# Kernel optimization log

Hardware: AMD Instinct MI355X
Metric: run time of the kernel (lower is better)

Reference implementation:

```python
import jax, jax.numpy as jnp
import numpy as np

N = 16384
E = 262144
IN_F, HID, ENC = 3, 128, 768
NEG_SLOPE = 0.2
EPS = 1e-5


def _glorot(key, shape):
    lim = float(np.sqrt(6.0 / (shape[0] + shape[1])))
    return jax.random.uniform(key, shape, jnp.float32, -lim, lim)


def layernorm(x, g, b):
    mu = jnp.mean(x, axis=-1, keepdims=True)
    var = jnp.mean(jnp.square(x - mu), axis=-1, keepdims=True)
    return (x - mu) * jax.lax.rsqrt(var + EPS) * g + b


def gatv2(x, src, dst, Wl, bl, Wr, br, att, bias, n_nodes):
    # single-head GATv2: message = lin_l(x)[src], score from lin_l(x)[src] + lin_r(x)[dst]
    xl = x @ Wl + bl                                  # [N, C]
    xr = x @ Wr + br                                  # [N, C]
    e = jax.nn.leaky_relu(xl[src] + xr[dst], NEG_SLOPE) @ att   # [E]
    m = jax.ops.segment_max(e, dst, num_segments=n_nodes)       # per-dst max (self-loops => no empty segs)
    ex = jnp.exp(e - m[dst])
    denom = jax.ops.segment_sum(ex, dst, num_segments=n_nodes)
    alpha = ex / denom[dst]                           # [E]
    out = jax.ops.segment_sum(alpha[:, None] * xl[src], dst, num_segments=n_nodes)
    return out + bias


def setup_inputs() -> dict:
    key = jax.random.key(0)
    ks = jax.random.split(key, 12)
    x = jax.random.normal(ks[0], (N, IN_F), jnp.float32)
    edge_index = jax.random.randint(ks[1], (2, E), 0, N, jnp.int64)
    return {
        "x": x,
        "edge_index": edge_index,
        "Wfc": _glorot(ks[2], (IN_F, ENC)),
        "bfc": jnp.zeros((ENC,), jnp.float32),
        "W1l": _glorot(ks[3], (IN_F, HID)),
        "b1l": jnp.zeros((HID,), jnp.float32),
        "W1r": _glorot(ks[4], (IN_F, HID)),
        "b1r": jnp.zeros((HID,), jnp.float32),
        "att1": _glorot(ks[5], (HID, 1))[:, 0],
        "bias1": jnp.zeros((HID,), jnp.float32),
        "g_bn1": jnp.ones((HID,), jnp.float32),
        "bb_bn1": jnp.zeros((HID,), jnp.float32),
        "W2l": _glorot(ks[6], (HID, ENC)),
        "b2l": jnp.zeros((ENC,), jnp.float32),
        "W2r": _glorot(ks[7], (HID, ENC)),
        "b2r": jnp.zeros((ENC,), jnp.float32),
        "att2": _glorot(ks[8], (ENC, 1))[:, 0],
        "bias2": jnp.zeros((ENC,), jnp.float32),
        "g_norm": jnp.ones((ENC,), jnp.float32),
        "b_norm": jnp.zeros((ENC,), jnp.float32),
    }


def reference(x, edge_index, Wfc, bfc, W1l, b1l, W1r, b1r, att1, bias1,
              g_bn1, bb_bn1, W2l, b2l, W2r, b2r, att2, bias2, g_norm, b_norm):
    loops = jnp.arange(N, dtype=edge_index.dtype)
    src = jnp.concatenate([edge_index[0], loops])   # add self-loops (PyG default)
    dst = jnp.concatenate([edge_index[1], loops])
    res = x @ Wfc + bfc                              # [N, ENC]
    h = gatv2(x, src, dst, W1l, b1l, W1r, b1r, att1, bias1, N)
    h = jax.nn.elu(layernorm(h, g_bn1, bb_bn1))
    h = gatv2(h, src, dst, W2l, b2l, W2r, b2r, att2, bias2, N)
    return layernorm(h + res, g_norm, b_norm)
```

## Files before the change

kernel.cpp:

```cpp
#include <hip/hip_runtime.h>

#define N_NODES 16384
#define N_EDGES 262144
#define EP (N_EDGES + N_NODES)
#define HID 128
#define ENC 768
#define ENCP (ENC/2)
#define EPSV 1e-5f

typedef unsigned short u16;
typedef unsigned char u8;
using f32x4  = __attribute__((ext_vector_type(4))) float;
using bf16x8 = __attribute__((ext_vector_type(8))) short;
using v2f    = __attribute__((ext_vector_type(2))) float;

__device__ __forceinline__ float wave_sum(float v){
  #pragma unroll
  for(int m=32;m>=1;m>>=1) v += __shfl_xor(v, m, 64);
  return v;
}
__device__ __forceinline__ unsigned bf16rtne(float f){
  const unsigned u = __float_as_uint(f);
  return (u + 0x7fffu + ((u>>16)&1u)) >> 16;
}
__device__ __forceinline__ unsigned pack2(float a, float b){
  return bf16rtne(a) | (bf16rtne(b) << 16);
}
__device__ __forceinline__ float bf2f(u16 h){ return __uint_as_float(((unsigned)h) << 16); }
__device__ __forceinline__ float plo(unsigned u){ return __uint_as_float(u << 16); }
__device__ __forceinline__ float phi(unsigned u){ return __uint_as_float(u & 0xffff0000u); }
__device__ __forceinline__ u8 f2fp8(float v){
  return (u8)(__builtin_amdgcn_cvt_pk_fp8_f32(v, v, 0, false) & 0xff);
}

#define LIN1_BLKS (N_NODES/4)
#define WPREP_BLKS (2*ENC*HID/256)
#define HIST_BLKS (EP/256)
#define W2A_BLKS 258
__global__ __launch_bounds__(256) void prep_kernel(
    const float* __restrict__ x,
    const float* __restrict__ W1l, const float* __restrict__ b1l,
    const float* __restrict__ W1r, const float* __restrict__ b1r,
    const float* __restrict__ att1,
    const float* __restrict__ W2l, const float* __restrict__ W2r,
    const float* __restrict__ b2l, const float* __restrict__ b2r,
    const float* __restrict__ att2,
    const int* __restrict__ ei,
    unsigned* __restrict__ xl1p, unsigned* __restrict__ xr1p,
    float* __restrict__ dotl1, float* __restrict__ dotr1,
    u16* __restrict__ Wtb, float* __restrict__ w2a,
    int* __restrict__ hist){
  const int bid = blockIdx.x;
  if(bid < LIN1_BLKS){
    const int lane = threadIdx.x & 63;
    const int n = bid*4 + (threadIdx.x >> 6);
    const float x0 = x[n*3], x1 = x[n*3+1], x2 = x[n*3+2];
    const int c0 = lane, c1 = lane + 64;
    const float la = x0*W1l[c0] + x1*W1l[HID+c0] + x2*W1l[2*HID+c0] + b1l[c0];
    const float lb = x0*W1l[c1] + x1*W1l[HID+c1] + x2*W1l[2*HID+c1] + b1l[c1];
    const float ra = x0*W1r[c0] + x1*W1r[HID+c0] + x2*W1r[2*HID+c0] + b1r[c0];
    const float rb = x0*W1r[c1] + x1*W1r[HID+c1] + x2*W1r[2*HID+c1] + b1r[c1];
    const float aa = att1[c0], ab = att1[c1];
    const float dl = wave_sum(la*aa + lb*ab);
    const float dr = wave_sum(ra*aa + rb*ab);
    if(lane == 0){ dotl1[n] = 0.6f*dl; dotr1[n] = 0.6f*dr; }
    xl1p[n*64+lane] = pack2(la, lb);
    xr1p[n*64+lane] = pack2(ra, rb);
  } else if(bid < LIN1_BLKS + WPREP_BLKS){
    const int idx = (bid - LIN1_BLKS)*256 + threadIdx.x;
    const int n = idx >> 7, k = idx & 127;
    const float v = (n < ENC) ? W2l[k*ENC + n] : W2r[k*ENC + (n-ENC)];
    Wtb[idx] = (u16)bf16rtne(v);
  } else if(bid < LIN1_BLKS + WPREP_BLKS + HIST_BLKS){
    const int i = (bid - LIN1_BLKS - WPREP_BLKS)*256 + threadIdx.x;
    const int dst = (i < N_EDGES) ? ei[N_EDGES + i] : (i - N_EDGES);
    atomicAdd(&hist[dst], 1);
  } else {
    const int idx = bid - (LIN1_BLKS + WPREP_BLKS + HIST_BLKS);
    const float* src = (idx < 128) ? (W2l + (size_t)idx*ENC)
                     : (idx < 256) ? (W2r + (size_t)(idx-128)*ENC)
                     : (idx == 256) ? b2l : b2r;
    float partial = 0.f;
    for(int c = threadIdx.x; c < ENC; c += 256) partial += src[c]*att2[c];
    partial = wave_sum(partial);
    __shared__ float red4[4];
    if((threadIdx.x & 63) == 0) red4[threadIdx.x >> 6] = partial;
    __syncthreads();
    if(threadIdx.x == 0) w2a[idx] = red4[0]+red4[1]+red4[2]+red4[3];
  }
}

__global__ __launch_bounds__(1024) void scan_kernel(
    const int* __restrict__ hist, int* __restrict__ rowstart){
  __shared__ int sums[1024];
  const int t = threadIdx.x;
  const int base = t*16;
  int loc[16];
  int s = 0;
  #pragma unroll
  for(int i=0;i<16;i++){ loc[i] = s; s += hist[base+i]; }
  sums[t] = s;
  __syncthreads();
  for(int off=1; off<1024; off<<=1){
    int v = 0;
    if(t >= off) v = sums[t-off];
    __syncthreads();
    if(t >= off) sums[t] += v;
    __syncthreads();
  }
  const int prev = (t==0) ? 0 : sums[t-1];
  #pragma unroll
  for(int i=0;i<16;i++) rowstart[base+i] = prev + loc[i];
  if(t == 1023) rowstart[N_NODES] = EP;
}

__global__ __launch_bounds__(256) void scatter_kernel(
    const int* __restrict__ ei, const int* __restrict__ rowstart,
    int* __restrict__ cursor, int* __restrict__ ssrc){
  const int i = blockIdx.x*256 + threadIdx.x;
  const int src = (i < N_EDGES) ? ei[i]           : (i - N_EDGES);
  const int dst = (i < N_EDGES) ? ei[N_EDGES + i] : (i - N_EDGES);
  const int pos = rowstart[dst] + atomicAdd(&cursor[dst], 1);
  ssrc[pos] = src;
}

__global__ __launch_bounds__(256) void node1_kernel(
    const unsigned* __restrict__ xl1p, const unsigned* __restrict__ xr1p,
    const float* __restrict__ att1,
    const float* __restrict__ dotl1, const float* __restrict__ dotr1,
    const float* __restrict__ bias1,
    const float* __restrict__ g1, const float* __restrict__ b1,
    const float* __restrict__ w2a,
    const int* __restrict__ rowstart, const int* __restrict__ ssrc,
    u16* __restrict__ h1b, unsigned* __restrict__ h1p,
    float* __restrict__ dotl2, float* __restrict__ dotr2){
  const int lane = threadIdx.x & 63;
  const int n = blockIdx.x*4 + (threadIdx.x >> 6);
  const unsigned xru = xr1p[n*64 + lane];
  const float xra = plo(xru), xrb = phi(xru);
  const float sa = 0.4f*att1[lane], sb = 0.4f*att1[lane+64];
  const float ebase = dotr1[n];
  float acc0 = 0.f, acc1 = 0.f, denom = 0.f;
  int p = rowstart[n];
  const int p1 = rowstart[n+1];
  for(; p+1 < p1; p += 2){
    const int s0 = ssrc[p], s1 = ssrc[p+1];
    const unsigned u0 = xl1p[s0*64 + lane];
    const unsigned u1 = xl1p[s1*64 + lane];
    const float dl0 = dotl1[s0], dl1 = dotl1[s1];
    const float a0 = plo(u0), b0 = phi(u0);
    const float a1 = plo(u1), b1v = phi(u1);
    float q0 = fmaf(sa, __builtin_fabsf(a0+xra), sb*__builtin_fabsf(b0+xrb));
    float q1 = fmaf(sa, __builtin_fabsf(a1+xra), sb*__builtin_fabsf(b1v+xrb));
    #pragma unroll
    for(int m=32;m>=1;m>>=1){
      q0 += __shfl_xor(q0, m, 64);
      q1 += __shfl_xor(q1, m, 64);
    }
    const float w0 = __expf(q0 + dl0 + ebase), w1 = __expf(q1 + dl1 + ebase);
    denom += w0 + w1;
    acc0 += w0*a0 + w1*a1;
    acc1 += w0*b0 + w1*b1v;
  }
  if(p < p1){
    const int s0 = ssrc[p];
    const unsigned u0 = xl1p[s0*64 + lane];
    const float a0 = plo(u0), b0 = phi(u0);
    const float q = wave_sum(fmaf(sa, __builtin_fabsf(a0+xra), sb*__builtin_fabsf(b0+xrb)));
    const float w0 = __expf(q + dotl1[s0] + ebase);
    denom += w0; acc0 += w0*a0; acc1 += w0*b0;
  }
  const float inv = 1.f/denom;
  const float y0 = acc0*inv + bias1[lane];
  const float y1 = acc1*inv + bias1[lane+64];
  const float mu  = wave_sum(y0+y1) * (1.f/HID);
  const float d0 = y0-mu, d1 = y1-mu;
  const float var = wave_sum(d0*d0 + d1*d1) * (1.f/HID);
  const float r = rsqrtf(var + EPSV);
  float z0 = d0*r*g1[lane] + b1[lane];
  float z1 = d1*r*g1[lane+64] + b1[lane+64];
  z0 = z0 > 0.f ? z0 : expm1f(z0);
  z1 = z1 > 0.f ? z1 : expm1f(z1);
  h1b[n*HID+lane]    = (u16)bf16rtne(z0);
  h1b[n*HID+lane+64] = (u16)bf16rtne(z1);
  h1p[n*64+lane]     = pack2(z0, z1);
  float dl2 = z0*w2a[lane]     + z1*w2a[lane+64];
  float dr2 = z0*w2a[128+lane] + z1*w2a[128+lane+64];
  #pragma unroll
  for(int m=32;m>=1;m>>=1){
    dl2 += __shfl_xor(dl2, m, 64);
    dr2 += __shfl_xor(dr2, m, 64);
  }
  if(lane == 0){
    dotl2[n] = 0.6f*(dl2 + w2a[256]);
    dotr2[n] = 0.6f*(dr2 + w2a[257]);
  }
}

#define LBM 128
#define LBN 128
__global__ __launch_bounds__(256) void mfma_lin2_kernel(
    const u16* __restrict__ h1b, const u16* __restrict__ Wtb,
    const float* __restrict__ b2l, const float* __restrict__ b2r,
    u8* __restrict__ xl8, u16* __restrict__ xr2u){
  __shared__ __align__(16) u16 Cs[LBM*128];
  const int t = threadIdx.x;
  const int mb = blockIdx.x * LBM;
  const int nb = blockIdx.y * LBN;
  const int w = t >> 6, lane = t & 63;
  const int l15 = lane & 15, g = lane >> 4;
  const int ar0 = mb + w*32 + l15, ar1 = ar0 + 16;
  bf16x8 a0[4], a1[4];
  #pragma unroll
  for(int ks=0;ks<4;ks++){
    a0[ks] = *(const bf16x8*)(h1b + (size_t)ar0*128 + ks*32 + g*8);
    a1[ks] = *(const bf16x8*)(h1b + (size_t)ar1*128 + ks*32 + g*8);
  }
  f32x4 acc0[8], acc1[8];
  #pragma unroll
  for(int j=0;j<8;j++){ acc0[j]=(f32x4){0,0,0,0}; acc1[j]=(f32x4){0,0,0,0}; }
  #pragma unroll
  for(int j=0;j<8;j++){
    const int brn = nb + j*16 + l15;
    #pragma unroll
    for(int ks=0;ks<4;ks++){
      const bf16x8 b = *(const bf16x8*)(Wtb + (size_t)brn*128 + ks*32 + g*8);
      acc0[j] = __builtin_amdgcn_mfma_f32_16x16x32_bf16(a0[ks], b, acc0[j], 0,0,0);
      acc1[j] = __builtin_amdgcn_mfma_f32_16x16x32_bf16(a1[ks], b, acc1[j], 0,0,0);
    }
  }
  if(nb < ENC){
    u8* Cs8 = (u8*)Cs;
    float biasj[8];
    #pragma unroll
    for(int j=0;j<8;j++) biasj[j] = b2l[nb + j*16 + l15];
    #pragma unroll
    for(int j=0;j<8;j++){
      const int col = j*16 + l15;
      #pragma unroll
      for(int r4=0;r4<4;r4++){
        const int row0 = w*32 + g*4 + r4;
        Cs8[row0*128 + (col ^ ((row0&7)<<4))] = f2fp8(acc0[j][r4] + biasj[j]);
        const int row1 = row0 + 16;
        Cs8[row1*128 + (col ^ ((row1&7)<<4))] = f2fp8(acc1[j][r4] + biasj[j]);
      }
    }
    __syncthreads();
    #pragma unroll
    for(int idx=t; idx<LBM*8; idx+=256){
      const int row = idx >> 3, ch = idx & 7;
      const uint4 v = *(const uint4*)(Cs8 + row*128 + ((ch*16) ^ ((row&7)<<4)));
      *(uint4*)(xl8 + (size_t)(mb+row)*ENC + nb + ch*16) = v;
    }
  } else {
    const float* bsrc = b2r + (nb - ENC);
    float biasj[8];
    #pragma unroll
    for(int j=0;j<8;j++) biasj[j] = bsrc[j*16 + l15];
    #pragma unroll
    for(int j=0;j<8;j++){
      const int coll = j*16 + l15;
      #pragma unroll
      for(int r4=0;r4<4;r4++){
        const int row0 = w*32 + g*4 + r4;
        *(u16*)((char*)Cs + row0*256 + ((coll*2) ^ ((row0&7)<<4))) =
            (u16)bf16rtne(acc0[j][r4] + biasj[j]);
        const int row1 = row0 + 16;
        *(u16*)((char*)Cs + row1*256 + ((coll*2) ^ ((row1&7)<<4))) =
            (u16)bf16rtne(acc1[j][r4] + biasj[j]);
      }
    }
    __syncthreads();
    u16* dst0 = xr2u + (nb - ENC);
    const int rr = t >> 4, cc = t & 15;
    #pragma unroll
    for(int it=0; it<8; ++it){
      const int row = it*16 + rr;
      const uint4 v = *(const uint4*)((const char*)Cs + row*256 + ((cc*16) ^ ((row&7)<<4)));
      *(uint4*)(dst0 + (size_t)(mb+row)*ENC + cc*8) = v;
    }
  }
}

__global__ __launch_bounds__(256) void node2b_kernel(
    const u8* __restrict__ xl8, const unsigned* __restrict__ xr2b,
    const float* __restrict__ att2,
    const float* __restrict__ dotl2, const float* __restrict__ dotr2,
    const unsigned* __restrict__ h1p,
    const int* __restrict__ rowstart, const int* __restrict__ ssrc,
    u16* __restrict__ aggb){
  const int lane = threadIdx.x & 63;
  const int n = blockIdx.x*4 + (threadIdx.x >> 6);
  const uint2* xrrow = (const uint2*)(xr2b + (size_t)n*ENCP);
  float xr[12], sg[12];
  #pragma unroll
  for(int k=0;k<3;k++){
    const uint2 u = xrrow[lane + 64*k];
    xr[4*k]   = plo(u.x); xr[4*k+1] = phi(u.x);
    xr[4*k+2] = plo(u.y); xr[4*k+3] = phi(u.y);
    const int cb = 4*(lane + 64*k);
    sg[4*k]   = 0.4f*att2[cb];   sg[4*k+1] = 0.4f*att2[cb+1];
    sg[4*k+2] = 0.4f*att2[cb+2]; sg[4*k+3] = 0.4f*att2[cb+3];
  }
  const float ebase = dotr2[n];
  float denom = 0.f, acc0 = 0.f, acc1 = 0.f;
  int p = rowstart[n];
  const int p1 = rowstart[n+1];
  for(; p+1 < p1; p += 2){
    const int s0 = ssrc[p], s1 = ssrc[p+1];
    const unsigned* r0 = (const unsigned*)(xl8 + (size_t)s0*ENC);
    const unsigned* r1 = (const unsigned*)(xl8 + (size_t)s1*ENC);
    unsigned v0[3], v1[3];
    #pragma unroll
    for(int k=0;k<3;k++){ v0[k] = r0[lane + 64*k]; v1[k] = r1[lane + 64*k]; }
    const float dl0 = dotl2[s0], dl1 = dotl2[s1];
    const unsigned hu0 = h1p[s0*64 + lane];
    const unsigned hu1 = h1p[s1*64 + lane];
    float q0 = 0.f, q1 = 0.f;
    #pragma unroll
    for(int k=0;k<3;k++){
      const v2f f01 = __builtin_amdgcn_cvt_pk_f32_fp8(v0[k], false);
      const v2f f23 = __builtin_amdgcn_cvt_pk_f32_fp8(v0[k], true);
      q0 = fmaf(sg[4*k],   __builtin_fabsf(f01.x+xr[4*k]),   q0);
      q0 = fmaf(sg[4*k+1], __builtin_fabsf(f01.y+xr[4*k+1]), q0);
      q0 = fmaf(sg[4*k+2], __builtin_fabsf(f23.x+xr[4*k+2]), q0);
      q0 = fmaf(sg[4*k+3], __builtin_fabsf(f23.y+xr[4*k+3]), q0);
      const v2f g01 = __builtin_amdgcn_cvt_pk_f32_fp8(v1[k], false);
      const v2f g23 = __builtin_amdgcn_cvt_pk_f32_fp8(v1[k], true);
      q1 = fmaf(sg[4*k],   __builtin_fabsf(g01.x+xr[4*k]),   q1);
      q1 = fmaf(sg[4*k+1], __builtin_fabsf(g01.y+xr[4*k+1]), q1);
      q1 = fmaf(sg[4*k+2], __builtin_fabsf(g23.x+xr[4*k+2]), q1);
      q1 = fmaf(sg[4*k+3], __builtin_fabsf(g23.y+xr[4*k+3]), q1);
    }
    #pragma unroll
    for(int m=32;m>=1;m>>=1){
      q0 += __shfl_xor(q0, m, 64);
      q1 += __shfl_xor(q1, m, 64);
    }
    const float w0 = __expf(q0 + dl0 + ebase), w1 = __expf(q1 + dl1 + ebase);
    denom += w0 + w1;
    acc0 += w0*plo(hu0) + w1*plo(hu1);
    acc1 += w0*phi(hu0) + w1*phi(hu1);
  }
  if(p < p1){
    const int s0 = ssrc[p];
    const unsigned* r0 = (const unsigned*)(xl8 + (size_t)s0*ENC);
    float q0 = 0.f;
    #pragma unroll
    for(int k=0;k<3;k++){
      const unsigned v = r0[lane + 64*k];
      const v2f f01 = __builtin_amdgcn_cvt_pk_f32_fp8(v, false);
      const v2f f23 = __builtin_amdgcn_cvt_pk_f32_fp8(v, true);
      q0 = fmaf(sg[4*k],   __builtin_fabsf(f01.x+xr[4*k]),   q0);
      q0 = fmaf(sg[4*k+1], __builtin_fabsf(f01.y+xr[4*k+1]), q0);
      q0 = fmaf(sg[4*k+2], __builtin_fabsf(f23.x+xr[4*k+2]), q0);
      q0 = fmaf(sg[4*k+3], __builtin_fabsf(f23.y+xr[4*k+3]), q0);
    }
    const unsigned hu0 = h1p[s0*64 + lane];
    const float w0 = __expf(wave_sum(q0) + dotl2[s0] + ebase);
    denom += w0; acc0 += w0*plo(hu0); acc1 += w0*phi(hu0);
  }
  const float inv = 1.f/denom;
  aggb[n*HID+lane]    = (u16)bf16rtne(acc0*inv);
  aggb[n*HID+lane+64] = (u16)bf16rtne(acc1*inv);
}

#define YSTR 770
__global__ __launch_bounds__(256) void gemm3_mfma_kernel(
    const u16* __restrict__ aggb, const u16* __restrict__ Wtb,
    const float* __restrict__ b2l, const float* __restrict__ bias2,
    const float* __restrict__ x, const float* __restrict__ Wfc,
    const float* __restrict__ bfc,
    const float* __restrict__ gn, const float* __restrict__ bn,
    float* __restrict__ out){
  __shared__ u16 Ys[64*YSTR];
  __shared__ float cbs[ENC];
  __shared__ float wfs[3][ENC];
  __shared__ float mus[64], rss[64];
  const int t = threadIdx.x;
  const int mb = blockIdx.x * 64;
  for(int c=t; c<ENC; c+=256){
    cbs[c] = b2l[c] + bias2[c] + bfc[c];
    wfs[0][c] = Wfc[c]; wfs[1][c] = Wfc[ENC+c]; wfs[2][c] = Wfc[2*ENC+c];
  }
  const int w = t >> 6, lane = t & 63;
  const int l15 = lane & 15, g = lane >> 4;
  const int ar = mb + w*16 + l15;
  bf16x8 a[4];
  #pragma unroll
  for(int ks=0;ks<4;ks++)
    a[ks] = *(const bf16x8*)(aggb + (size_t)ar*128 + ks*32 + g*8);
  float xv0[4], xv1[4], xv2[4];
  #pragma unroll
  for(int r4=0;r4<4;r4++){
    const int rrow = mb + w*16 + g*4 + r4;
    xv0[r4] = x[rrow*3]; xv1[r4] = x[rrow*3+1]; xv2[r4] = x[rrow*3+2];
  }
  float rs[4] = {0,0,0,0}, rq[4] = {0,0,0,0};
  __syncthreads();
  #pragma unroll
  for(int sub=0; sub<6; ++sub){
    const int nb = sub*128;
    f32x4 acc[8];
    #pragma unroll
    for(int j=0;j<8;j++) acc[j]=(f32x4){0,0,0,0};
    #pragma unroll
    for(int j=0;j<8;j++){
      const int brn = nb + j*16 + l15;
      #pragma unroll
      for(int ks=0;ks<4;ks++){
        const bf16x8 b = *(const bf16x8*)(Wtb + (size_t)brn*128 + ks*32 + g*8);
        acc[j] = __builtin_amdgcn_mfma_f32_16x16x32_bf16(a[ks], b, acc[j], 0,0,0);
      }
    }
    #pragma unroll
    for(int j=0;j<8;j++){
      const int col = nb + j*16 + l15;
      const float cb = cbs[col];
      const float w0 = wfs[0][col], w1 = wfs[1][col], w2 = wfs[2][col];
      #pragma unroll
      for(int r4=0;r4<4;r4++){
        const int lrow = w*16 + g*4 + r4;
        const float y = acc[j][r4] + cb + xv0[r4]*w0 + xv1[r4]*w1 + xv2[r4]*w2;
        rs[r4] += y; rq[r4] += y*y;
        Ys[lrow*YSTR + col] = (u16)bf16rtne(y);
      }
    }
  }
  #pragma unroll
  for(int m=8;m>=1;m>>=1){
    #pragma unroll
    for(int r4=0;r4<4;r4++){
      rs[r4] += __shfl_xor(rs[r4], m, 64);
      rq[r4] += __shfl_xor(rq[r4], m, 64);
    }
  }
  if(l15 == 0){
    #pragma unroll
    for(int r4=0;r4<4;r4++){
      const int lrow = w*16 + g*4 + r4;
      const float mu = rs[r4] * (1.f/ENC);
      const float var = rq[r4] * (1.f/ENC) - mu*mu;
      mus[lrow] = mu;
      rss[lrow] = rsqrtf(var + EPSV);
    }
  }
  __syncthreads();
  float gv[12], bv[12];
  #pragma unroll
  for(int j2=0;j2<12;j2++){ gv[j2] = gn[lane + j2*64]; bv[j2] = bn[lane + j2*64]; }
  for(int r=0; r<16; ++r){
    const int lrow = w*16 + r;
    const float mu = mus[lrow], rstd = rss[lrow];
    float* orow = out + (size_t)(mb+lrow)*ENC;
    #pragma unroll
    for(int j2=0;j2<12;j2++){
      const float y = bf2f(Ys[lrow*YSTR + lane + j2*64]);
      orow[lane + j2*64] = (y - mu)*rstd*gv[j2] + bv[j2];
    }
  }
}

extern "C" void kernel_launch(void* const* d_in, const int* in_sizes, int n_in,
                              void* d_out, int out_size, void* d_ws, size_t ws_size,
                              hipStream_t stream) {
  const float* x    = (const float*)d_in[0];
  const int*   ei   = (const int*)  d_in[1];
  const float* Wfc  = (const float*)d_in[2];
  const float* bfc  = (const float*)d_in[3];
  const float* W1l  = (const float*)d_in[4];
  const float* b1l  = (const float*)d_in[5];
  const float* W1r  = (const float*)d_in[6];
  const float* b1r  = (const float*)d_in[7];
  const float* att1 = (const float*)d_in[8];
  const float* bias1= (const float*)d_in[9];
  const float* g1   = (const float*)d_in[10];
  const float* bb1  = (const float*)d_in[11];
  const float* W2l  = (const float*)d_in[12];
  const float* b2l  = (const float*)d_in[13];
  const float* W2r  = (const float*)d_in[14];
  const float* b2r  = (const float*)d_in[15];
  const float* att2 = (const float*)d_in[16];
  const float* bias2= (const float*)d_in[17];
  const float* gn   = (const float*)d_in[18];
  const float* bn   = (const float*)d_in[19];
  float* out = (float*)d_out;

  char* w = (char*)d_ws;
  auto alloc = [&](size_t bytes){ void* p = (void*)w; w += (bytes + 255) & ~(size_t)255; return p; };
  int*      hist     = (int*)     alloc((size_t)N_NODES*4);
  int*      cursor   = (int*)     alloc((size_t)N_NODES*4);
  int*      rowstart = (int*)     alloc((size_t)(N_NODES+1)*4);
  int*      ssrc     = (int*)     alloc((size_t)EP*4);
  unsigned* xl1p     = (unsigned*)alloc((size_t)N_NODES*64*4);
  unsigned* xr1p     = (unsigned*)alloc((size_t)N_NODES*64*4);
  float*    dotl1    = (float*)   alloc((size_t)N_NODES*4);
  float*    dotr1    = (float*)   alloc((size_t)N_NODES*4);
  float*    dotl2    = (float*)   alloc((size_t)N_NODES*4);
  float*    dotr2    = (float*)   alloc((size_t)N_NODES*4);
  u16*      h1b      = (u16*)     alloc((size_t)N_NODES*HID*2);
  unsigned* h1p      = (unsigned*)alloc((size_t)N_NODES*64*4);
  u16*      aggb     = (u16*)     alloc((size_t)N_NODES*HID*2);
  u8*       xl8      = (u8*)      alloc((size_t)N_NODES*ENC);
  unsigned* xr2b     = (unsigned*)alloc((size_t)N_NODES*ENCP*4);
  u16*      Wtb      = (u16*)     alloc((size_t)2*ENC*HID*2);
  float*    w2a      = (float*)   alloc((size_t)W2A_BLKS*4);

  hipMemsetAsync(hist, 0, (size_t)N_NODES*8, stream);

  prep_kernel<<<LIN1_BLKS+WPREP_BLKS+HIST_BLKS+W2A_BLKS, 256, 0, stream>>>(
      x, W1l, b1l, W1r, b1r, att1, W2l, W2r, b2l, b2r, att2, ei,
      xl1p, xr1p, dotl1, dotr1, Wtb, w2a, hist);
  scan_kernel<<<1, 1024, 0, stream>>>(hist, rowstart);
  scatter_kernel<<<EP/256, 256, 0, stream>>>(ei, rowstart, cursor, ssrc);
  node1_kernel<<<N_NODES/4, 256, 0, stream>>>(xl1p, xr1p, att1, dotl1, dotr1,
                                              bias1, g1, bb1, w2a,
                                              rowstart, ssrc, h1b, h1p, dotl2, dotr2);
  mfma_lin2_kernel<<<dim3(N_NODES/LBM, 2*ENC/LBN), 256, 0, stream>>>(
      h1b, Wtb, b2l, b2r, xl8, (u16*)xr2b);
  node2b_kernel<<<N_NODES/4, 256, 0, stream>>>(xl8, xr2b, att2, dotl2, dotr2,
                                               h1p, rowstart, ssrc, aggb);
  gemm3_mfma_kernel<<<N_NODES/64, 256, 0, stream>>>(aggb, Wtb, b2l, bias2,
                                                    x, Wfc, bfc, gn, bn, out);
}
```

Baseline: 192.7 us.

## Split GAT layers into per-edge score kernels and per-node aggregation kernels

Replaces the wave-per-node attention loops with a thread-per-edge score kernel that computes each edge's exp-weight serially over the feature dimension, then separate per-node aggregation kernels. Layer 1 aggregation is rewritten algebraically to aggregate the 3-dim raw inputs and apply W1l afterwards (linearity), removing the 128-wide gather. Edges are packed as src|dst<<14 so score kernels can find both endpoints. Costs extra kernel launches, edge-weight buffers, and uncoalesced per-thread row loads (768 fp8 + bf16 per edge) in score2.

```diff
diff --git a/kernel.cpp b/kernel.cpp
--- a/kernel.cpp
+++ b/kernel.cpp
@@ -5,7 +5,6 @@
 #define EP (N_EDGES + N_NODES)
 #define HID 128
 #define ENC 768
-#define ENCP (ENC/2)
 #define EPSV 1e-5f
 
 typedef unsigned short u16;
@@ -32,6 +31,18 @@
 __device__ __forceinline__ u8 f2fp8(float v){
   return (u8)(__builtin_amdgcn_cvt_pk_fp8_f32(v, v, 0, false) & 0xff);
 }
+
+#define CH2(ad, bd, sx, sy, q) { \
+  q = fmaf(sx, __builtin_fabsf(plo(ad)+plo(bd)), q); \
+  q = fmaf(sy, __builtin_fabsf(phi(ad)+phi(bd)), q); }
+
+#define DWX(ax, blo, bhi, s4, q) { \
+  const v2f A01 = __builtin_amdgcn_cvt_pk_f32_fp8(ax, false); \
+  const v2f A23 = __builtin_amdgcn_cvt_pk_f32_fp8(ax, true);  \
+  q = fmaf(s4.x, __builtin_fabsf(A01.x+plo(blo)), q); \
+  q = fmaf(s4.y, __builtin_fabsf(A01.y+phi(blo)), q); \
+  q = fmaf(s4.z, __builtin_fabsf(A23.x+plo(bhi)), q); \
+  q = fmaf(s4.w, __builtin_fabsf(A23.y+phi(bhi)), q); }
 
 #define LIN1_BLKS (N_NODES/4)
 #define WPREP_BLKS (2*ENC*HID/256)
@@ -46,7 +57,8 @@
     const float* __restrict__ b2l, const float* __restrict__ b2r,
     const float* __restrict__ att2,
     const int* __restrict__ ei,
-    unsigned* __restrict__ xl1p, unsigned* __restrict__ xr1p,
+    u16* __restrict__ xl1b, u16* __restrict__ xr1b,
+    float4* __restrict__ xpad,
     float* __restrict__ dotl1, float* __restrict__ dotr1,
     u16* __restrict__ Wtb, float* __restrict__ w2a,
     int* __restrict__ hist){
@@ -63,9 +75,12 @@
     const float aa = att1[c0], ab = att1[c1];
     const float dl = wave_sum(la*aa + lb*ab);
     const float dr = wave_sum(ra*aa + rb*ab);
-    if(lane == 0){ dotl1[n] = 0.6f*dl; dotr1[n] = 0.6f*dr; }
-    xl1p[n*64+lane] = pack2(la, lb);
-    xr1p[n*64+lane] = pack2(ra, rb);
+    if(lane == 0){
+      dotl1[n] = 0.6f*dl; dotr1[n] = 0.6f*dr;
+      xpad[n] = make_float4(x0, x1, x2, 0.f);
+    }
+    xl1b[n*HID+c0] = (u16)bf16rtne(la); xl1b[n*HID+c1] = (u16)bf16rtne(lb);
+    xr1b[n*HID+c0] = (u16)bf16rtne(ra); xr1b[n*HID+c1] = (u16)bf16rtne(rb);
   } else if(bid < LIN1_BLKS + WPREP_BLKS){
     const int idx = (bid - LIN1_BLKS)*256 + threadIdx.x;
     const int n = idx >> 7, k = idx & 127;
@@ -116,74 +131,83 @@
 
 __global__ __launch_bounds__(256) void scatter_kernel(
     const int* __restrict__ ei, const int* __restrict__ rowstart,
-    int* __restrict__ cursor, int* __restrict__ ssrc){
+    int* __restrict__ cursor, unsigned* __restrict__ sedge){
   const int i = blockIdx.x*256 + threadIdx.x;
   const int src = (i < N_EDGES) ? ei[i]           : (i - N_EDGES);
   const int dst = (i < N_EDGES) ? ei[N_EDGES + i] : (i - N_EDGES);
   const int pos = rowstart[dst] + atomicAdd(&cursor[dst], 1);
-  ssrc[pos] = src;
-}
-
-__global__ __launch_bounds__(256) void node1_kernel(
-    const unsigned* __restrict__ xl1p, const unsigned* __restrict__ xr1p,
+  sedge[pos] = (unsigned)src | ((unsigned)dst << 14);
+}
+
+__global__ __launch_bounds__(256) void score1_kernel(
+    const u16* __restrict__ xl1b, const u16* __restrict__ xr1b,
     const float* __restrict__ att1,
     const float* __restrict__ dotl1, const float* __restrict__ dotr1,
+    const unsigned* __restrict__ sedge, float* __restrict__ w1){
+  __shared__ __align__(16) float sg[HID];
+  const int t = threadIdx.x;
+  if(t < HID) sg[t] = 0.4f*att1[t];
+  __syncthreads();
+  const int p = blockIdx.x*256 + t;
+  const unsigned v = sedge[p];
+  const int s = v & 16383, d = v >> 14;
+  const uint4* A = (const uint4*)(xl1b + (size_t)s*HID);
+  const uint4* B = (const uint4*)(xr1b + (size_t)d*HID);
+  const float4* S4 = (const float4*)sg;
+  float q0=0.f,q1=0.f,q2=0.f,q3=0.f;
+  #pragma unroll
+  for(int k=0;k<16;k++){
+    const uint4 a = A[k], b = B[k];
+    const float4 s0 = S4[2*k], s1 = S4[2*k+1];
+    CH2(a.x,b.x,s0.x,s0.y,q0) CH2(a.y,b.y,s0.z,s0.w,q1)
+    CH2(a.z,b.z,s1.x,s1.y,q2) CH2(a.w,b.w,s1.z,s1.w,q3)
+  }
+  w1[p] = __expf(q0+q1+q2+q3 + dotl1[s] + dotr1[d]);
+}
+
+__global__ __launch_bounds__(256) void agg1_kernel(
+    const unsigned* __restrict__ sedge, const float* __restrict__ w1,
+    const float4* __restrict__ xpad, const int* __restrict__ rowstart,
+    float4* __restrict__ agg4){
+  const int n = blockIdx.x*256 + threadIdx.x;
+  const int p1 = rowstart[n+1];
+  float a0=0.f,a1=0.f,a2=0.f,dn=0.f;
+  for(int p=rowstart[n]; p<p1; ++p){
+    const unsigned v = sedge[p];
+    const float w = w1[p];
+    const float4 xv = xpad[v & 16383];
+    a0 += w*xv.x; a1 += w*xv.y; a2 += w*xv.z; dn += w;
+  }
+  agg4[n] = make_float4(a0,a1,a2,dn);
+}
+
+__global__ __launch_bounds__(256) void h1lin_kernel(
+    const float4* __restrict__ agg4,
+    const float* __restrict__ W1l, const float* __restrict__ b1l,
     const float* __restrict__ bias1,
     const float* __restrict__ g1, const float* __restrict__ b1,
     const float* __restrict__ w2a,
-    const int* __restrict__ rowstart, const int* __restrict__ ssrc,
     u16* __restrict__ h1b, unsigned* __restrict__ h1p,
     float* __restrict__ dotl2, float* __restrict__ dotr2){
   const int lane = threadIdx.x & 63;
   const int n = blockIdx.x*4 + (threadIdx.x >> 6);
-  const unsigned xru = xr1p[n*64 + lane];
-  const float xra = plo(xru), xrb = phi(xru);
-  const float sa = 0.4f*att1[lane], sb = 0.4f*att1[lane+64];
-  const float ebase = dotr1[n];
-  float acc0 = 0.f, acc1 = 0.f, denom = 0.f;
-  int p = rowstart[n];
-  const int p1 = rowstart[n+1];
-  for(; p+1 < p1; p += 2){
-    const int s0 = ssrc[p], s1 = ssrc[p+1];
-    const unsigned u0 = xl1p[s0*64 + lane];
-    const unsigned u1 = xl1p[s1*64 + lane];
-    const float dl0 = dotl1[s0], dl1 = dotl1[s1];
-    const float a0 = plo(u0), b0 = phi(u0);
-    const float a1 = plo(u1), b1v = phi(u1);
-    float q0 = fmaf(sa, __builtin_fabsf(a0+xra), sb*__builtin_fabsf(b0+xrb));
-    float q1 = fmaf(sa, __builtin_fabsf(a1+xra), sb*__builtin_fabsf(b1v+xrb));
-    #pragma unroll
-    for(int m=32;m>=1;m>>=1){
-      q0 += __shfl_xor(q0, m, 64);
-      q1 += __shfl_xor(q1, m, 64);
-    }
-    const float w0 = __expf(q0 + dl0 + ebase), w1 = __expf(q1 + dl1 + ebase);
-    denom += w0 + w1;
-    acc0 += w0*a0 + w1*a1;
-    acc1 += w0*b0 + w1*b1v;
-  }
-  if(p < p1){
-    const int s0 = ssrc[p];
-    const unsigned u0 = xl1p[s0*64 + lane];
-    const float a0 = plo(u0), b0 = phi(u0);
-    const float q = wave_sum(fmaf(sa, __builtin_fabsf(a0+xra), sb*__builtin_fabsf(b0+xrb)));
-    const float w0 = __expf(q + dotl1[s0] + ebase);
-    denom += w0; acc0 += w0*a0; acc1 += w0*b0;
-  }
-  const float inv = 1.f/denom;
-  const float y0 = acc0*inv + bias1[lane];
-  const float y1 = acc1*inv + bias1[lane+64];
+  const float4 ag = agg4[n];
+  const float inv = 1.f/ag.w;
+  const float a0 = ag.x*inv, a1 = ag.y*inv, a2 = ag.z*inv;
+  const int c0 = lane, c1 = lane + 64;
+  const float y0 = a0*W1l[c0] + a1*W1l[HID+c0] + a2*W1l[2*HID+c0] + b1l[c0] + bias1[c0];
+  const float y1 = a0*W1l[c1] + a1*W1l[HID+c1] + a2*W1l[2*HID+c1] + b1l[c1] + bias1[c1];
   const float mu  = wave_sum(y0+y1) * (1.f/HID);
   const float d0 = y0-mu, d1 = y1-mu;
   const float var = wave_sum(d0*d0 + d1*d1) * (1.f/HID);
   const float r = rsqrtf(var + EPSV);
-  float z0 = d0*r*g1[lane] + b1[lane];
-  float z1 = d1*r*g1[lane+64] + b1[lane+64];
+  float z0 = d0*r*g1[c0] + b1[c0];
+  float z1 = d1*r*g1[c1] + b1[c1];
   z0 = z0 > 0.f ? z0 : expm1f(z0);
   z1 = z1 > 0.f ? z1 : expm1f(z1);
-  h1b[n*HID+lane]    = (u16)bf16rtne(z0);
-  h1b[n*HID+lane+64] = (u16)bf16rtne(z1);
-  h1p[n*64+lane]     = pack2(z0, z1);
+  h1b[n*HID+c0] = (u16)bf16rtne(z0);
+  h1b[n*HID+c1] = (u16)bf16rtne(z1);
+  h1p[n*64+lane] = pack2(z0, z1);
   float dl2 = z0*w2a[lane]     + z1*w2a[lane+64];
   float dr2 = z0*w2a[128+lane] + z1*w2a[128+lane+64];
   #pragma unroll
@@ -282,83 +306,61 @@
   }
 }
 
-__global__ __launch_bounds__(256) void node2b_kernel(
-    const u8* __restrict__ xl8, const unsigned* __restrict__ xr2b,
+__global__ __launch_bounds__(256) void score2_kernel(
+    const u8* __restrict__ xl8, const u16* __restrict__ xr2u,
     const float* __restrict__ att2,
     const float* __restrict__ dotl2, const float* __restrict__ dotr2,
-    const unsigned* __restrict__ h1p,
-    const int* __restrict__ rowstart, const int* __restrict__ ssrc,
+    const unsigned* __restrict__ sedge, float* __restrict__ w2){
+  __shared__ __align__(16) float sg[ENC];
+  const int t = threadIdx.x;
+  for(int c=t; c<ENC; c+=256) sg[c] = 0.4f*att2[c];
+  __syncthreads();
+  const int p = blockIdx.x*256 + t;
+  const unsigned v = sedge[p];
+  const int s = v & 16383, d = v >> 14;
+  const uint4* A = (const uint4*)(xl8 + (size_t)s*ENC);
+  const uint4* B = (const uint4*)(xr2u + (size_t)d*ENC);
+  const float4* S4 = (const float4*)sg;
+  float q0=0.f,q1=0.f,q2=0.f,q3=0.f;
+  #pragma unroll 4
+  for(int k=0;k<48;k++){
+    const uint4 a = A[k];
+    const uint4 b0 = B[2*k], b1 = B[2*k+1];
+    const float4 s0 = S4[4*k], s1 = S4[4*k+1], s2 = S4[4*k+2], s3 = S4[4*k+3];
+    DWX(a.x, b0.x, b0.y, s0, q0)
+    DWX(a.y, b0.z, b0.w, s1, q1)
+    DWX(a.z, b1.x, b1.y, s2, q2)
+    DWX(a.w, b1.z, b1.w, s3, q3)
+  }
+  w2[p] = __expf(q0+q1+q2+q3 + dotl2[s] + dotr2[d]);
+}
+
+__global__ __launch_bounds__(256) void agg2_kernel(
+    const unsigned* __restrict__ sedge, const float* __restrict__ w2,
+    const unsigned* __restrict__ h1p, const int* __restrict__ rowstart,
     u16* __restrict__ aggb){
   const int lane = threadIdx.x & 63;
   const int n = blockIdx.x*4 + (threadIdx.x >> 6);
-  const uint2* xrrow = (const uint2*)(xr2b + (size_t)n*ENCP);
-  float xr[12], sg[12];
-  #pragma unroll
-  for(int k=0;k<3;k++){
-    const uint2 u = xrrow[lane + 64*k];
-    xr[4*k]   = plo(u.x); xr[4*k+1] = phi(u.x);
-    xr[4*k+2] = plo(u.y); xr[4*k+3] = phi(u.y);
-    const int cb = 4*(lane + 64*k);
-    sg[4*k]   = 0.4f*att2[cb];   sg[4*k+1] = 0.4f*att2[cb+1];
-    sg[4*k+2] = 0.4f*att2[cb+2]; sg[4*k+3] = 0.4f*att2[cb+3];
-  }
-  const float ebase = dotr2[n];
-  float denom = 0.f, acc0 = 0.f, acc1 = 0.f;
+  float denom=0.f, acc0=0.f, acc1=0.f;
   int p = rowstart[n];
   const int p1 = rowstart[n+1];
-  for(; p+1 < p1; p += 2){
-    const int s0 = ssrc[p], s1 = ssrc[p+1];
-    const unsigned* r0 = (const unsigned*)(xl8 + (size_t)s0*ENC);
-    const unsigned* r1 = (const unsigned*)(xl8 + (size_t)s1*ENC);
-    unsigned v0[3], v1[3];
-    #pragma unroll
-    for(int k=0;k<3;k++){ v0[k] = r0[lane + 64*k]; v1[k] = r1[lane + 64*k]; }
-    const float dl0 = dotl2[s0], dl1 = dotl2[s1];
-    const unsigned hu0 = h1p[s0*64 + lane];
-    const unsigned hu1 = h1p[s1*64 + lane];
-    float q0 = 0.f, q1 = 0.f;
-    #pragma unroll
-    for(int k=0;k<3;k++){
-      const v2f f01 = __builtin_amdgcn_cvt_pk_f32_fp8(v0[k], false);
-      const v2f f23 = __builtin_amdgcn_cvt_pk_f32_fp8(v0[k], true);
-      q0 = fmaf(sg[4*k],   __builtin_fabsf(f01.x+xr[4*k]),   q0);
-      q0 = fmaf(sg[4*k+1], __builtin_fabsf(f01.y+xr[4*k+1]), q0);
-      q0 = fmaf(sg[4*k+2], __builtin_fabsf(f23.x+xr[4*k+2]), q0);
-      q0 = fmaf(sg[4*k+3], __builtin_fabsf(f23.y+xr[4*k+3]), q0);
-      const v2f g01 = __builtin_amdgcn_cvt_pk_f32_fp8(v1[k], false);
-      const v2f g23 = __builtin_amdgcn_cvt_pk_f32_fp8(v1[k], true);
-      q1 = fmaf(sg[4*k],   __builtin_fabsf(g01.x+xr[4*k]),   q1);
-      q1 = fmaf(sg[4*k+1], __builtin_fabsf(g01.y+xr[4*k+1]), q1);
-      q1 = fmaf(sg[4*k+2], __builtin_fabsf(g23.x+xr[4*k+2]), q1);
-      q1 = fmaf(sg[4*k+3], __builtin_fabsf(g23.y+xr[4*k+3]), q1);
-    }
-    #pragma unroll
-    for(int m=32;m>=1;m>>=1){
-      q0 += __shfl_xor(q0, m, 64);
-      q1 += __shfl_xor(q1, m, 64);
-    }
-    const float w0 = __expf(q0 + dl0 + ebase), w1 = __expf(q1 + dl1 + ebase);
-    denom += w0 + w1;
-    acc0 += w0*plo(hu0) + w1*plo(hu1);
-    acc1 += w0*phi(hu0) + w1*phi(hu1);
-  }
-  if(p < p1){
-    const int s0 = ssrc[p];
-    const unsigned* r0 = (const unsigned*)(xl8 + (size_t)s0*ENC);
-    float q0 = 0.f;
-    #pragma unroll
-    for(int k=0;k<3;k++){
-      const unsigned v = r0[lane + 64*k];
-      const v2f f01 = __builtin_amdgcn_cvt_pk_f32_fp8(v, false);
-      const v2f f23 = __builtin_amdgcn_cvt_pk_f32_fp8(v, true);
-      q0 = fmaf(sg[4*k],   __builtin_fabsf(f01.x+xr[4*k]),   q0);
-      q0 = fmaf(sg[4*k+1], __builtin_fabsf(f01.y+xr[4*k+1]), q0);
-      q0 = fmaf(sg[4*k+2], __builtin_fabsf(f23.x+xr[4*k+2]), q0);
-      q0 = fmaf(sg[4*k+3], __builtin_fabsf(f23.y+xr[4*k+3]), q0);
-    }
-    const unsigned hu0 = h1p[s0*64 + lane];
-    const float w0 = __expf(wave_sum(q0) + dotl2[s0] + ebase);
-    denom += w0; acc0 += w0*plo(hu0); acc1 += w0*phi(hu0);
+  for(; p+3 < p1; p += 4){
+    const unsigned v0 = sedge[p],   v1 = sedge[p+1];
+    const unsigned v2 = sedge[p+2], v3 = sedge[p+3];
+    const float w0 = w2[p], w1v = w2[p+1], w2v = w2[p+2], w3 = w2[p+3];
+    const unsigned h0 = h1p[(v0 & 16383)*64 + lane];
+    const unsigned h1 = h1p[(v1 & 16383)*64 + lane];
+    const unsigned h2 = h1p[(v2 & 16383)*64 + lane];
+    const unsigned h3 = h1p[(v3 & 16383)*64 + lane];
+    denom += (w0+w1v) + (w2v+w3);
+    acc0 += w0*plo(h0) + w1v*plo(h1) + w2v*plo(h2) + w3*plo(h3);
+    acc1 += w0*phi(h0) + w1v*phi(h1) + w2v*phi(h2) + w3*phi(h3);
+  }
+  for(; p < p1; ++p){
+    const unsigned v = sedge[p];
+    const float w = w2[p];
+    const unsigned h = h1p[(v & 16383)*64 + lane];
+    denom += w; acc0 += w*plo(h); acc1 += w*phi(h);
   }
   const float inv = 1.f/denom;
   aggb[n*HID+lane]    = (u16)bf16rtne(acc0*inv);
@@ -491,18 +493,22 @@
   int*      hist     = (int*)     alloc((size_t)N_NODES*4);
   int*      cursor   = (int*)     alloc((size_t)N_NODES*4);
   int*      rowstart = (int*)     alloc((size_t)(N_NODES+1)*4);
-  int*      ssrc     = (int*)     alloc((size_t)EP*4);
-  unsigned* xl1p     = (unsigned*)alloc((size_t)N_NODES*64*4);
-  unsigned* xr1p     = (unsigned*)alloc((size_t)N_NODES*64*4);
+  unsigned* sedge    = (unsigned*)alloc((size_t)EP*4);
+  u16*      xl1b     = (u16*)     alloc((size_t)N_NODES*HID*2);
+  u16*      xr1b     = (u16*)     alloc((size_t)N_NODES*HID*2);
+  float4*   xpad     = (float4*)  alloc((size_t)N_NODES*16);
   float*    dotl1    = (float*)   alloc((size_t)N_NODES*4);
   float*    dotr1    = (float*)   alloc((size_t)N_NODES*4);
   float*    dotl2    = (float*)   alloc((size_t)N_NODES*4);
   float*    dotr2    = (float*)   alloc((size_t)N_NODES*4);
+  float*    w1       = (float*)   alloc((size_t)EP*4);
+  float*    w2       = (float*)   alloc((size_t)EP*4);
+  float4*   agg4     = (float4*)  alloc((size_t)N_NODES*16);
   u16*      h1b      = (u16*)     alloc((size_t)N_NODES*HID*2);
   unsigned* h1p      = (unsigned*)alloc((size_t)N_NODES*64*4);
   u16*      aggb     = (u16*)     alloc((size_t)N_NODES*HID*2);
   u8*       xl8      = (u8*)      alloc((size_t)N_NODES*ENC);
-  unsigned* xr2b     = (unsigned*)alloc((size_t)N_NODES*ENCP*4);
+  u16*      xr2u     = (u16*)     alloc((size_t)N_NODES*ENC*2);
   u16*      Wtb      = (u16*)     alloc((size_t)2*ENC*HID*2);
   float*    w2a      = (float*)   alloc((size_t)W2A_BLKS*4);
 
@@ -510,16 +516,19 @@
 
   prep_kernel<<<LIN1_BLKS+WPREP_BLKS+HIST_BLKS+W2A_BLKS, 256, 0, stream>>>(
       x, W1l, b1l, W1r, b1r, att1, W2l, W2r, b2l, b2r, att2, ei,
-      xl1p, xr1p, dotl1, dotr1, Wtb, w2a, hist);
+      xl1b, xr1b, xpad, dotl1, dotr1, Wtb, w2a, hist);
   scan_kernel<<<1, 1024, 0, stream>>>(hist, rowstart);
-  scatter_kernel<<<EP/256, 256, 0, stream>>>(ei, rowstart, cursor, ssrc);
-  node1_kernel<<<N_NODES/4, 256, 0, stream>>>(xl1p, xr1p, att1, dotl1, dotr1,
-                                              bias1, g1, bb1, w2a,
-                                              rowstart, ssrc, h1b, h1p, dotl2, dotr2);
+  scatter_kernel<<<EP/256, 256, 0, stream>>>(ei, rowstart, cursor, sedge);
+  score1_kernel<<<EP/256, 256, 0, stream>>>(xl1b, xr1b, att1, dotl1, dotr1,
+                                            sedge, w1);
+  agg1_kernel<<<N_NODES/256, 256, 0, stream>>>(sedge, w1, xpad, rowstart, agg4);
+  h1lin_kernel<<<N_NODES/4, 256, 0, stream>>>(agg4, W1l, b1l, bias1, g1, bb1,
+                                              w2a, h1b, h1p, dotl2, dotr2);
   mfma_lin2_kernel<<<dim3(N_NODES/LBM, 2*ENC/LBN), 256, 0, stream>>>(
-      h1b, Wtb, b2l, b2r, xl8, (u16*)xr2b);
-  node2b_kernel<<<N_NODES/4, 256, 0, stream>>>(xl8, xr2b, att2, dotl2, dotr2,
-                                               h1p, rowstart, ssrc, aggb);
+      h1b, Wtb, b2l, b2r, xl8, xr2u);
+  score2_kernel<<<EP/256, 256, 0, stream>>>(xl8, xr2u, att2, dotl2, dotr2,
+                                            sedge, w2);
+  agg2_kernel<<<N_NODES/4, 256, 0, stream>>>(sedge, w2, h1p, rowstart, aggb);
   gemm3_mfma_kernel<<<N_NODES/64, 256, 0, stream>>>(aggb, Wtb, b2l, bias2,
                                                     x, Wfc, bfc, gn, bn, out);
 }
```

New measurement: 248.1 us. 1.29x slower.
